# Kernel optimization log

Measured on AMD Instinct MI355X. Metric: run time of the kernel, lower is better.

Reference implementation:

```python
import jax, jax.numpy as jnp
import numpy as np

B, S, E = 2, 2048, 1024
D_ATTN, H = 1024, 16
HD = D_ATTN // H
SCALE = 1.0 / np.sqrt(D_ATTN)
ROPE_BASE = 10000.0


def setup_inputs() -> dict:
    key = jax.random.key(0)
    ks = jax.random.split(key, 7)
    def w(k, shape, scale):
        return jax.random.normal(k, shape, dtype=jnp.float32) * scale
    return {
        "q": w(ks[0], (B, S, E), 1.0),
        "k": w(ks[1], (B, S, E), 1.0),
        "v": w(ks[2], (B, S, E), 1.0),
        "Wq": w(ks[3], (D_ATTN, E), E ** -0.5),
        "Wk": w(ks[4], (D_ATTN, E), E ** -0.5),
        "Wv": w(ks[5], (D_ATTN, E), E ** -0.5),
        "Wo": w(ks[6], (E, D_ATTN), D_ATTN ** -0.5),
    }


def _rope(x):
    # x: [B, H, S, HD]; interleaved-pair rotary embedding over the seq axis
    s, d = x.shape[2], x.shape[3]
    half = d // 2
    inv_freq = 1.0 / (ROPE_BASE ** (jnp.arange(half, dtype=jnp.float32) * 2.0 / d))
    ang = jnp.arange(s, dtype=jnp.float32)[:, None] * inv_freq[None, :]  # [S, half]
    cos, sin = jnp.cos(ang), jnp.sin(ang)
    xr = x.reshape(x.shape[:-1] + (half, 2))
    x0, x1 = xr[..., 0], xr[..., 1]
    o0 = x0 * cos - x1 * sin
    o1 = x0 * sin + x1 * cos
    return jnp.stack([o0, o1], axis=-1).reshape(x.shape)


def reference(q, k, v, Wq, Wk, Wv, Wo):
    # linear projections (nn.Linear with weight [out, in]): y = x @ W^T
    qh = (q @ Wq.T).reshape(B, S, H, HD).transpose(0, 2, 1, 3)  # [B,H,S,HD]
    kh = (k @ Wk.T).reshape(B, S, H, HD).transpose(0, 2, 1, 3)
    vh = (v @ Wv.T).reshape(B, S, H, HD).transpose(0, 2, 1, 3)
    qh = _rope(qh)
    kh = _rope(kh)
    # shifted-causal mask: disallow j >= i (diagonal masked), except (0,0) allowed
    i = jnp.arange(S)[:, None]
    j = jnp.arange(S)[None, :]
    masked = j >= i                              # triu incl. diagonal
    masked = masked.at[0, 0].set(False)          # keep (0,0) so row 0 isn't all -inf
    scores = jnp.einsum("bhsd,bhtd->bhst", qh, kh) * SCALE
    scores = jnp.where(masked, -jnp.inf, scores)
    probs = jax.nn.softmax(scores, axis=-1)      # dropout omitted (eval mode)
    ctx = jnp.einsum("bhst,bhtd->bhsd", probs, vh)
    ctx = ctx.transpose(0, 2, 1, 3).reshape(B, S, D_ATTN)
    return ctx @ Wo.T
```

## Files before the change

### kernel.cpp

```cpp
#include <hip/hip_runtime.h>
#include <hip/hip_bf16.h>

#define BATCH 2
#define SEQ   2048
#define EMB   1024
#define DATTN 1024
#define NH    16
#define HD    64
#define MM    (BATCH*SEQ)
#define SCALE 0.03125f
#define MINIT -1.0e30f
#define ROPE_COEF 0.41524101186f

using bf16x8 = __attribute__((ext_vector_type(8))) short;
using f32x4  = __attribute__((ext_vector_type(4))) float;

__device__ inline short f2bf(float x) {
    __hip_bfloat16 b = __float2bfloat16(x);
    return *reinterpret_cast<short*>(&b);
}

__device__ inline void gl_lds16(const short* g, short* l) {
    __builtin_amdgcn_global_load_lds(
        (const __attribute__((address_space(1))) unsigned int*)g,
        (__attribute__((address_space(3))) unsigned int*)l, 16, 0, 0);
}

__global__ __launch_bounds__(256)
void cvt_all(const float* __restrict__ q, const float* __restrict__ k,
             const float* __restrict__ v,
             const float* __restrict__ Wq, const float* __restrict__ Wk,
             const float* __restrict__ Wv, const float* __restrict__ Wo,
             short* __restrict__ dst)
{
    const long QKV = (long)MM * EMB;
    const long WSZ = (long)DATTN * EMB;
    const long i = ((long)blockIdx.x * 256 + threadIdx.x) * 4;
    const float* s;
    long off;
    if (i < 3 * QKV) {
        const int seg = (int)(i / QKV);
        off = i - (long)seg * QKV;
        s = (seg == 0) ? q : (seg == 1) ? k : v;
    } else {
        const long j = i - 3 * QKV;
        const int seg = (int)(j / WSZ);
        off = j - (long)seg * WSZ;
        s = (seg == 0) ? Wq : (seg == 1) ? Wk : (seg == 2) ? Wv : Wo;
    }
    float4 x = *(const float4*)(s + off);
    short4 y;
    y.x = f2bf(x.x); y.y = f2bf(x.y); y.z = f2bf(x.z); y.w = f2bf(x.w);
    *(short4*)(dst + i) = y;
}

__device__ inline void stage_tile(const short* g, short* lds, int wave, int lane) {
    #pragma unroll
    for (int qq = 0; qq < 2; ++qq) {
        const int r = wave * 32 + qq * 16 + (lane >> 2);
        gl_lds16(g + (long)r * EMB + (lane & 3) * 8, lds + (wave * 2 + qq) * 512);
    }
}

__global__ __launch_bounds__(256)
void gemm_proj_bf16(const short* __restrict__ qb, const short* __restrict__ kb,
                    const short* __restrict__ vb,
                    const short* __restrict__ wqb, const short* __restrict__ wkb,
                    const short* __restrict__ wvb,
                    short* __restrict__ Qb, short* __restrict__ Kb,
                    short* __restrict__ Vtb)
{
    const short* A; const short* B;
    if (blockIdx.z == 0)      { A = qb; B = wqb; }
    else if (blockIdx.z == 1) { A = kb; B = wkb; }
    else                      { A = vb; B = wvb; }

    __shared__ short sA[128 * 32];
    __shared__ short sB[128 * 32];

    const int tid  = threadIdx.x;
    const int wave = tid >> 6, lane = tid & 63;
    const int quad = lane >> 4, l16 = lane & 15;
    const int wm = (wave >> 1) * 64, wn = (wave & 1) * 64;
    const long m0 = (long)blockIdx.x * 128, n0 = (long)blockIdx.y * 128;

    f32x4 acc[4][4];
    #pragma unroll
    for (int i = 0; i < 4; ++i)
        #pragma unroll
        for (int j = 0; j < 4; ++j) acc[i][j] = (f32x4){0.f, 0.f, 0.f, 0.f};

    for (int kt = 0; kt < EMB; kt += 32) {
        __syncthreads();
        stage_tile(A + m0 * EMB + kt, sA, wave, lane);
        stage_tile(B + n0 * EMB + kt, sB, wave, lane);
        __syncthreads();

        bf16x8 af[4], bfr[4];
        #pragma unroll
        for (int rt = 0; rt < 4; ++rt)
            af[rt] = *(const bf16x8*)&sA[(wm + rt * 16 + l16) * 32 + quad * 8];
        #pragma unroll
        for (int ct = 0; ct < 4; ++ct)
            bfr[ct] = *(const bf16x8*)&sB[(wn + ct * 16 + l16) * 32 + quad * 8];
        #pragma unroll
        for (int rt = 0; rt < 4; ++rt)
            #pragma unroll
            for (int ct = 0; ct < 4; ++ct)
                acc[rt][ct] = __builtin_amdgcn_mfma_f32_16x16x32_bf16(
                    af[rt], bfr[ct], acc[rt][ct], 0, 0, 0);
    }

    if (blockIdx.z < 2) {
        short* C = (blockIdx.z == 0) ? Qb : Kb;
        const float scl = (blockIdx.z == 0) ? SCALE : 1.0f;
        const int odd = l16 & 1;
        #pragma unroll
        for (int ct = 0; ct < 4; ++ct) {
            const long col = n0 + wn + ct * 16 + l16;
            const int hh = (int)(col >> 6), dd = (int)(col & (HD - 1));
            const float invf = exp2f(-ROPE_COEF * (float)(dd >> 1));
            #pragma unroll
            for (int rt = 0; rt < 4; ++rt) {
                #pragma unroll
                for (int reg = 0; reg < 4; ++reg) {
                    const long row = m0 + wm + rt * 16 + quad * 4 + reg;
                    const int bb = (int)(row >> 11), ss = (int)(row & (SEQ - 1));
                    const float val = acc[rt][ct][reg];
                    const float prt = __shfl_xor(val, 1, 64);
                    float sn, cs;
                    __sincosf((float)ss * invf, &sn, &cs);
                    const float o = odd ? (prt * sn + val * cs)
                                        : (val * cs - prt * sn);
                    C[(((long)(bb * NH + hh)) << 17) + ((long)ss << 6) + dd] =
                        f2bf(o * scl);
                }
            }
        }
    } else {
        #pragma unroll
        for (int rt = 0; rt < 4; ++rt) {
            #pragma unroll
            for (int ct = 0; ct < 4; ++ct) {
                const long row0 = m0 + wm + rt * 16 + quad * 4;
                const long col  = n0 + wn + ct * 16 + l16;
                const int bb = (int)(row0 >> 11), ss = (int)(row0 & (SEQ - 1));
                const int hh = (int)(col >> 6),   dd = (int)(col & (HD - 1));
                short4 s4;
                s4.x = f2bf(acc[rt][ct][0]); s4.y = f2bf(acc[rt][ct][1]);
                s4.z = f2bf(acc[rt][ct][2]); s4.w = f2bf(acc[rt][ct][3]);
                *(short4*)&Vtb[(((long)(bb * NH + hh)) << 17) + ((long)dd << 11) + ss] = s4;
            }
        }
    }
}

__global__ __launch_bounds__(256)
void gemm_out_bf16(const short* __restrict__ Ab, const short* __restrict__ Bb,
                   float* __restrict__ C)
{
    __shared__ short sA[128 * 32];
    __shared__ short sB[64 * 32];

    const int tid  = threadIdx.x;
    const int wave = tid >> 6, lane = tid & 63;
    const int quad = lane >> 4, l16 = lane & 15;
    const int wm = (wave >> 1) * 64, wn = (wave & 1) * 32;
    const long m0 = (long)blockIdx.x * 128, n0 = (long)blockIdx.y * 64;

    f32x4 acc[4][2];
    #pragma unroll
    for (int i = 0; i < 4; ++i)
        #pragma unroll
        for (int j = 0; j < 2; ++j) acc[i][j] = (f32x4){0.f, 0.f, 0.f, 0.f};

    for (int kt = 0; kt < DATTN; kt += 32) {
        __syncthreads();
        stage_tile(Ab + m0 * DATTN + kt, sA, wave, lane);
        gl_lds16(Bb + n0 * DATTN + kt
                     + (long)(wave * 16 + (lane >> 2)) * DATTN + (lane & 3) * 8,
                 sB + wave * 512);
        __syncthreads();

        bf16x8 af[4], bfr[2];
        #pragma unroll
        for (int rt = 0; rt < 4; ++rt)
            af[rt] = *(const bf16x8*)&sA[(wm + rt * 16 + l16) * 32 + quad * 8];
        #pragma unroll
        for (int ct = 0; ct < 2; ++ct)
            bfr[ct] = *(const bf16x8*)&sB[(wn + ct * 16 + l16) * 32 + quad * 8];
        #pragma unroll
        for (int rt = 0; rt < 4; ++rt)
            #pragma unroll
            for (int ct = 0; ct < 2; ++ct)
                acc[rt][ct] = __builtin_amdgcn_mfma_f32_16x16x32_bf16(
                    af[rt], bfr[ct], acc[rt][ct], 0, 0, 0);
    }

    #pragma unroll
    for (int rt = 0; rt < 4; ++rt) {
        #pragma unroll
        for (int ct = 0; ct < 2; ++ct) {
            #pragma unroll
            for (int reg = 0; reg < 4; ++reg) {
                const long row = m0 + wm + rt * 16 + quad * 4 + reg;
                const long col = n0 + wn + ct * 16 + l16;
                C[row * EMB + col] = acc[rt][ct][reg];
            }
        }
    }
}

#define KLD 64
#define PLD 72

__global__ __launch_bounds__(256, 2)
void flash_attn_mfma(const short* __restrict__ Qb,
                     const short* __restrict__ Kb,
                     const short* __restrict__ Vtb,
                     short* __restrict__ ctx)
{
    const int id  = blockIdx.x;
    const int hi  = id >> 8;
    const int idx = id & 255;
    const int r   = idx & 7;
    const int s5  = idx >> 3;
    const int pi  = s5 & 3;
    const int ts8 = s5 >> 2;
    const int p   = r + 8 * pi;
    const int b   = p >> 4, h = p & 15;
    const int t   = hi ? ts8 : (15 - ts8);

    const int tid = threadIdx.x;
    const int wave = tid >> 6, lane = tid & 63;
    const int quad = lane >> 4, l16 = lane & 15;
    const int r0 = t * 128;

    __shared__ short sk[2 * 64 * KLD];
    __shared__ short sv[2 * 64 * KLD];
    __shared__ short sp[4][32 * PLD];

    const long base = ((long)(b * NH + h)) << 17;

    const int iq0 = r0 + wave * 32 + l16;
    const int iq1 = iq0 + 16;
    const int dtile = 2 * t + (wave >> 1);
    const int rsw = l16 & 7;

    bf16x8 qf0[2], qf1[2];
    #pragma unroll
    for (int tt = 0; tt < 2; ++tt) {
        qf0[tt] = *(const bf16x8*)(Qb + base + (long)iq0 * HD + tt * 32 + quad * 8);
        qf1[tt] = *(const bf16x8*)(Qb + base + (long)iq1 * HD + tt * 32 + quad * 8);
    }

    f32x4 acc0[4], acc1[4];
    #pragma unroll
    for (int ct = 0; ct < 4; ++ct) {
        acc0[ct] = (f32x4){0.f, 0.f, 0.f, 0.f};
        acc1[ct] = (f32x4){0.f, 0.f, 0.f, 0.f};
    }
    float m0 = MINIT, l0 = 0.f;
    float m1 = MINIT, l1 = 0.f;

    const int njt = t + 1;

    #pragma unroll 1
    for (int jt = 0; jt < njt; ++jt) {
        const int jbase = jt * 128;

        __syncthreads();
        #pragma unroll
        for (int c = 0; c < 4; ++c) {
            const int cc   = c * 256 + tid;
            const int half = cc >> 9;
            const int row  = (cc >> 3) & 63;
            const int sch  = (cc & 7) ^ (row & 7);
            gl_lds16(Kb + base + (long)(jbase + half * 64 + row) * HD + sch * 8,
                     sk + ((c * 256 + wave * 64) << 3));
            gl_lds16(Vtb + base + ((long)row << 11) + jbase + half * 64 + sch * 8,
                     sv + ((c * 256 + wave * 64) << 3));
        }
        __syncthreads();

        #pragma unroll
        for (int half = 0; half < 2; ++half) {
            const int jt2 = 2 * jt + half;
            if (jt2 > dtile) continue;
            const int jb2 = jbase + half * 64;
            const short* skh = sk + half * 64 * KLD;
            const short* svh = sv + half * 64 * KLD;

            f32x4 s0[4], s1[4];
            __builtin_amdgcn_s_setprio(1);
            #pragma unroll
            for (int ct = 0; ct < 4; ++ct) {
                const int rr16 = (ct * 16 + l16) * KLD;
                bf16x8 k0 = *(const bf16x8*)&skh[rr16 + ((quad ^ rsw) << 3)];
                bf16x8 k1 = *(const bf16x8*)&skh[rr16 + (((4 + quad) ^ rsw) << 3)];
                f32x4 z0 = (f32x4){0.f, 0.f, 0.f, 0.f};
                z0 = __builtin_amdgcn_mfma_f32_16x16x32_bf16(k0, qf0[0], z0, 0, 0, 0);
                z0 = __builtin_amdgcn_mfma_f32_16x16x32_bf16(k1, qf0[1], z0, 0, 0, 0);
                s0[ct] = z0;
                f32x4 z1 = (f32x4){0.f, 0.f, 0.f, 0.f};
                z1 = __builtin_amdgcn_mfma_f32_16x16x32_bf16(k0, qf1[0], z1, 0, 0, 0);
                z1 = __builtin_amdgcn_mfma_f32_16x16x32_bf16(k1, qf1[1], z1, 0, 0, 0);
                s1[ct] = z1;
            }
            __builtin_amdgcn_s_setprio(0);

            if (jt2 == dtile) {
                #pragma unroll
                for (int ct = 0; ct < 4; ++ct)
                    #pragma unroll
                    for (int rr = 0; rr < 4; ++rr) {
                        const int j = jb2 + ct * 16 + quad * 4 + rr;
                        if (!((j < iq0) || (iq0 == 0 && j == 0)))
                            s0[ct][rr] = -INFINITY;
                        if (!(j < iq1))
                            s1[ct][rr] = -INFINITY;
                    }
            }

            float mx0 = MINIT;
            #pragma unroll
            for (int ct = 0; ct < 4; ++ct)
                #pragma unroll
                for (int rr = 0; rr < 4; ++rr) mx0 = fmaxf(mx0, s0[ct][rr]);
            mx0 = fmaxf(mx0, __shfl_xor(mx0, 16, 64));
            mx0 = fmaxf(mx0, __shfl_xor(mx0, 32, 64));
            const float mn0 = fmaxf(m0, mx0);
            const float a0 = __expf(m0 - mn0);
            m0 = mn0;
            float ss0 = 0.f;
            #pragma unroll
            for (int ct = 0; ct < 4; ++ct)
                #pragma unroll
                for (int rr = 0; rr < 4; ++rr) {
                    const float e = __expf(s0[ct][rr] - mn0);
                    s0[ct][rr] = e;
                    ss0 += e;
                }
            ss0 += __shfl_xor(ss0, 16, 64);
            ss0 += __shfl_xor(ss0, 32, 64);
            l0 = l0 * a0 + ss0;

            float mx1 = MINIT;
            #pragma unroll
            for (int ct = 0; ct < 4; ++ct)
                #pragma unroll
                for (int rr = 0; rr < 4; ++rr) mx1 = fmaxf(mx1, s1[ct][rr]);
            mx1 = fmaxf(mx1, __shfl_xor(mx1, 16, 64));
            mx1 = fmaxf(mx1, __shfl_xor(mx1, 32, 64));
            const float mn1 = fmaxf(m1, mx1);
            const float a1 = __expf(m1 - mn1);
            m1 = mn1;
            float ss1 = 0.f;
            #pragma unroll
            for (int ct = 0; ct < 4; ++ct)
                #pragma unroll
                for (int rr = 0; rr < 4; ++rr) {
                    const float e = __expf(s1[ct][rr] - mn1);
                    s1[ct][rr] = e;
                    ss1 += e;
                }
            ss1 += __shfl_xor(ss1, 16, 64);
            ss1 += __shfl_xor(ss1, 32, 64);
            l1 = l1 * a1 + ss1;

            short* pw0 = sp[wave];
            short* pw1 = sp[wave] + 16 * PLD;
            #pragma unroll
            for (int ct = 0; ct < 4; ++ct) {
                short4 p4;
                p4.x = f2bf(s0[ct][0]); p4.y = f2bf(s0[ct][1]);
                p4.z = f2bf(s0[ct][2]); p4.w = f2bf(s0[ct][3]);
                *(short4*)&pw0[l16 * PLD + ct * 16 + quad * 4] = p4;
                short4 q4;
                q4.x = f2bf(s1[ct][0]); q4.y = f2bf(s1[ct][1]);
                q4.z = f2bf(s1[ct][2]); q4.w = f2bf(s1[ct][3]);
                *(short4*)&pw1[l16 * PLD + ct * 16 + quad * 4] = q4;
            }

            #pragma unroll
            for (int ct = 0; ct < 4; ++ct)
                #pragma unroll
                for (int rr = 0; rr < 4; ++rr) {
                    acc0[ct][rr] *= a0;
                    acc1[ct][rr] *= a1;
                }

            bf16x8 pf00 = *(const bf16x8*)&pw0[l16 * PLD + quad * 8];
            bf16x8 pf01 = *(const bf16x8*)&pw0[l16 * PLD + 32 + quad * 8];
            bf16x8 pf10 = *(const bf16x8*)&pw1[l16 * PLD + quad * 8];
            bf16x8 pf11 = *(const bf16x8*)&pw1[l16 * PLD + 32 + quad * 8];

            __builtin_amdgcn_s_setprio(1);
            #pragma unroll
            for (int ct = 0; ct < 4; ++ct) {
                const int rr16 = (ct * 16 + l16) * KLD;
                bf16x8 v0 = *(const bf16x8*)&svh[rr16 + ((quad ^ rsw) << 3)];
                bf16x8 v1 = *(const bf16x8*)&svh[rr16 + (((4 + quad) ^ rsw) << 3)];
                acc0[ct] = __builtin_amdgcn_mfma_f32_16x16x32_bf16(
                    v0, pf00, acc0[ct], 0, 0, 0);
                acc0[ct] = __builtin_amdgcn_mfma_f32_16x16x32_bf16(
                    v1, pf01, acc0[ct], 0, 0, 0);
                acc1[ct] = __builtin_amdgcn_mfma_f32_16x16x32_bf16(
                    v0, pf10, acc1[ct], 0, 0, 0);
                acc1[ct] = __builtin_amdgcn_mfma_f32_16x16x32_bf16(
                    v1, pf11, acc1[ct], 0, 0, 0);
            }
            __builtin_amdgcn_s_setprio(0);
        }
    }

    {
        const float inv0 = 1.f / l0;
        short* orow = ctx + (long)(b * SEQ + iq0) * DATTN + h * HD;
        #pragma unroll
        for (int ct = 0; ct < 4; ++ct) {
            short4 o4;
            o4.x = f2bf(acc0[ct][0] * inv0);
            o4.y = f2bf(acc0[ct][1] * inv0);
            o4.z = f2bf(acc0[ct][2] * inv0);
            o4.w = f2bf(acc0[ct][3] * inv0);
            *(short4*)&orow[ct * 16 + quad * 4] = o4;
        }
    }
    {
        const float inv1 = 1.f / l1;
        short* orow = ctx + (long)(b * SEQ + iq1) * DATTN + h * HD;
        #pragma unroll
        for (int ct = 0; ct < 4; ++ct) {
            short4 o4;
            o4.x = f2bf(acc1[ct][0] * inv1);
            o4.y = f2bf(acc1[ct][1] * inv1);
            o4.z = f2bf(acc1[ct][2] * inv1);
            o4.w = f2bf(acc1[ct][3] * inv1);
            *(short4*)&orow[ct * 16 + quad * 4] = o4;
        }
    }
}

extern "C" void kernel_launch(void* const* d_in, const int* in_sizes, int n_in,
                              void* d_out, int out_size, void* d_ws, size_t ws_size,
                              hipStream_t stream) {
    const float* q  = (const float*)d_in[0];
    const float* k  = (const float*)d_in[1];
    const float* v  = (const float*)d_in[2];
    const float* Wq = (const float*)d_in[3];
    const float* Wk = (const float*)d_in[4];
    const float* Wv = (const float*)d_in[5];
    const float* Wo = (const float*)d_in[6];
    float* out = (float*)d_out;

    const long QKV = (long)MM * EMB;
    const long WSZ = (long)DATTN * EMB;
    short* basep = (short*)d_ws;
    short* qb  = basep;
    short* kb  = qb + QKV;
    short* vb  = kb + QKV;
    short* wqb = vb + QKV;
    short* wkb = wqb + WSZ;
    short* wvb = wkb + WSZ;
    short* wob = wvb + WSZ;
    short* Qb  = wob + WSZ;
    short* Kb  = Qb + QKV;
    short* Vtb = Kb + QKV;
    short* ctx = Vtb + QKV;

    cvt_all<<<16384, 256, 0, stream>>>(q, k, v, Wq, Wk, Wv, Wo, qb);

    gemm_proj_bf16<<<dim3(MM / 128, DATTN / 128, 3), 256, 0, stream>>>(
        qb, kb, vb, wqb, wkb, wvb, Qb, Kb, Vtb);

    flash_attn_mfma<<<512, 256, 0, stream>>>(Qb, Kb, Vtb, ctx);

    gemm_out_bf16<<<dim3(MM / 128, EMB / 64), 256, 0, stream>>>(ctx, wob, out);
}
```

Measured before the change: 222.4 us.

## Widen projection GEMM K-tile to 64 with swizzled LDS and transposed Q/K epilogue

The QKV projection GEMM now stages 64-wide K slices instead of 32, which halves the number of barrier-separated staging steps. The LDS layout uses an XOR swizzle to avoid bank conflicts on the 128-byte rows. For the Q and K outputs the MFMA operands are swapped so each lane holds four consecutive head-dim values. That lets the RoPE epilogue apply the rotation without cross-lane shuffles and store packed short4 vectors instead of scalar bf16 writes. LDS use per block doubles, which may reduce occupancy.

```diff
diff --git a/kernel.cpp b/kernel.cpp
--- a/kernel.cpp
+++ b/kernel.cpp
@@ -62,6 +62,17 @@
     }
 }
 
+__device__ inline void stage_tile64(const short* g, short* lds, int tid) {
+    #pragma unroll
+    for (int c = 0; c < 4; ++c) {
+        const int cc   = c * 256 + tid;
+        const int row  = cc >> 3;
+        const int slot = cc & 7;
+        const int ssl  = slot ^ (row & 7);
+        gl_lds16(g + (long)row * EMB + ssl * 8, lds + ((cc & ~63) << 3));
+    }
+}
+
 __global__ __launch_bounds__(256)
 void gemm_proj_bf16(const short* __restrict__ qb, const short* __restrict__ kb,
                     const short* __restrict__ vb,
@@ -74,15 +85,17 @@
     if (blockIdx.z == 0)      { A = qb; B = wqb; }
     else if (blockIdx.z == 1) { A = kb; B = wkb; }
     else                      { A = vb; B = wvb; }
-
-    __shared__ short sA[128 * 32];
-    __shared__ short sB[128 * 32];
+    const bool isv = (blockIdx.z == 2);
+
+    __shared__ short sA[128 * 64];
+    __shared__ short sB[128 * 64];
 
     const int tid  = threadIdx.x;
     const int wave = tid >> 6, lane = tid & 63;
     const int quad = lane >> 4, l16 = lane & 15;
     const int wm = (wave >> 1) * 64, wn = (wave & 1) * 64;
     const long m0 = (long)blockIdx.x * 128, n0 = (long)blockIdx.y * 128;
+    const int rsw = l16 & 7;
 
     f32x4 acc[4][4];
     #pragma unroll
@@ -90,51 +103,65 @@
         #pragma unroll
         for (int j = 0; j < 4; ++j) acc[i][j] = (f32x4){0.f, 0.f, 0.f, 0.f};
 
-    for (int kt = 0; kt < EMB; kt += 32) {
+    for (int kt = 0; kt < EMB; kt += 64) {
         __syncthreads();
-        stage_tile(A + m0 * EMB + kt, sA, wave, lane);
-        stage_tile(B + n0 * EMB + kt, sB, wave, lane);
+        stage_tile64(A + m0 * EMB + kt, sA, tid);
+        stage_tile64(B + n0 * EMB + kt, sB, tid);
         __syncthreads();
 
-        bf16x8 af[4], bfr[4];
-        #pragma unroll
-        for (int rt = 0; rt < 4; ++rt)
-            af[rt] = *(const bf16x8*)&sA[(wm + rt * 16 + l16) * 32 + quad * 8];
-        #pragma unroll
-        for (int ct = 0; ct < 4; ++ct)
-            bfr[ct] = *(const bf16x8*)&sB[(wn + ct * 16 + l16) * 32 + quad * 8];
-        #pragma unroll
-        for (int rt = 0; rt < 4; ++rt)
+        #pragma unroll
+        for (int kk = 0; kk < 2; ++kk) {
+            bf16x8 af[4], bfr[4];
+            #pragma unroll
+            for (int rt = 0; rt < 4; ++rt)
+                af[rt] = *(const bf16x8*)&sA[(wm + rt * 16 + l16) * 64
+                         + (((kk << 2) | quad) ^ rsw) * 8];
             #pragma unroll
             for (int ct = 0; ct < 4; ++ct)
-                acc[rt][ct] = __builtin_amdgcn_mfma_f32_16x16x32_bf16(
-                    af[rt], bfr[ct], acc[rt][ct], 0, 0, 0);
-    }
-
-    if (blockIdx.z < 2) {
+                bfr[ct] = *(const bf16x8*)&sB[(wn + ct * 16 + l16) * 64
+                          + (((kk << 2) | quad) ^ rsw) * 8];
+            if (isv) {
+                #pragma unroll
+                for (int i = 0; i < 4; ++i)
+                    #pragma unroll
+                    for (int j = 0; j < 4; ++j)
+                        acc[i][j] = __builtin_amdgcn_mfma_f32_16x16x32_bf16(
+                            af[i], bfr[j], acc[i][j], 0, 0, 0);
+            } else {
+                #pragma unroll
+                for (int i = 0; i < 4; ++i)
+                    #pragma unroll
+                    for (int j = 0; j < 4; ++j)
+                        acc[i][j] = __builtin_amdgcn_mfma_f32_16x16x32_bf16(
+                            bfr[i], af[j], acc[i][j], 0, 0, 0);
+            }
+        }
+    }
+
+    if (!isv) {
         short* C = (blockIdx.z == 0) ? Qb : Kb;
         const float scl = (blockIdx.z == 0) ? SCALE : 1.0f;
-        const int odd = l16 & 1;
-        #pragma unroll
-        for (int ct = 0; ct < 4; ++ct) {
-            const long col = n0 + wn + ct * 16 + l16;
-            const int hh = (int)(col >> 6), dd = (int)(col & (HD - 1));
-            const float invf = exp2f(-ROPE_COEF * (float)(dd >> 1));
-            #pragma unroll
-            for (int rt = 0; rt < 4; ++rt) {
-                #pragma unroll
-                for (int reg = 0; reg < 4; ++reg) {
-                    const long row = m0 + wm + rt * 16 + quad * 4 + reg;
-                    const int bb = (int)(row >> 11), ss = (int)(row & (SEQ - 1));
-                    const float val = acc[rt][ct][reg];
-                    const float prt = __shfl_xor(val, 1, 64);
-                    float sn, cs;
-                    __sincosf((float)ss * invf, &sn, &cs);
-                    const float o = odd ? (prt * sn + val * cs)
-                                        : (val * cs - prt * sn);
-                    C[(((long)(bb * NH + hh)) << 17) + ((long)ss << 6) + dd] =
-                        f2bf(o * scl);
-                }
+        #pragma unroll
+        for (int i = 0; i < 4; ++i) {
+            const int d0  = (int)(n0) + wn + i * 16 + quad * 4;
+            const int hh  = d0 >> 6, dd0 = d0 & (HD - 1);
+            const float invf0 = exp2f(-ROPE_COEF * (float)(dd0 >> 1));
+            const float invf1 = exp2f(-ROPE_COEF * (float)((dd0 >> 1) + 1));
+            #pragma unroll
+            for (int j = 0; j < 4; ++j) {
+                const int tok = (int)(m0) + wm + j * 16 + l16;
+                const int bb = tok >> 11, ss = tok & (SEQ - 1);
+                float s0, c0, s1, c1;
+                __sincosf((float)ss * invf0, &s0, &c0);
+                __sincosf((float)ss * invf1, &s1, &c1);
+                const f32x4 x = acc[i][j];
+                short4 o4;
+                o4.x = f2bf((x[0] * c0 - x[1] * s0) * scl);
+                o4.y = f2bf((x[0] * s0 + x[1] * c0) * scl);
+                o4.z = f2bf((x[2] * c1 - x[3] * s1) * scl);
+                o4.w = f2bf((x[2] * s1 + x[3] * c1) * scl);
+                *(short4*)&C[(((long)(bb * NH + hh)) << 17)
+                             + ((long)ss << 6) + dd0] = o4;
             }
         }
     } else {
```

Measured after the change: 214.4 us. 3.6% less time.
